# Kernel optimization log

Hardware: AMD Instinct MI355X
Metric: run time of the kernel (lower is better)

Reference implementation:

```python
import jax, jax.numpy as jnp
import numpy as np

N = 50000
E = 800000
IN_DIM = 128
HID = 32
HEADS = 4
NEG_SLOPE = 0.2


def setup_inputs() -> dict:
    key = jax.random.key(0)
    ks = jax.random.split(key, 12)
    x = jax.random.normal(ks[0], (N, IN_DIM), dtype=jnp.float32)
    edge_index = jax.random.randint(ks[1], (2, E), 0, N, dtype=jnp.int64)
    s1 = 1.0 / np.sqrt(IN_DIM)
    s2 = 1.0 / np.sqrt(HEADS * HID)
    W1 = jax.random.normal(ks[2], (IN_DIM, HEADS * HID), dtype=jnp.float32) * s1
    a_src1 = jax.random.normal(ks[3], (HEADS, HID), dtype=jnp.float32) * s1
    a_dst1 = jax.random.normal(ks[4], (HEADS, HID), dtype=jnp.float32) * s1
    b1 = jnp.zeros((HEADS * HID,), dtype=jnp.float32)
    W2 = jax.random.normal(ks[5], (HEADS * HID, HID), dtype=jnp.float32) * s2
    a_src2 = jax.random.normal(ks[6], (1, HID), dtype=jnp.float32) * s2
    a_dst2 = jax.random.normal(ks[7], (1, HID), dtype=jnp.float32) * s2
    b2 = jnp.zeros((HID,), dtype=jnp.float32)
    return {"x": x, "edge_index": edge_index, "W1": W1, "a_src1": a_src1,
            "a_dst1": a_dst1, "b1": b1, "W2": W2, "a_src2": a_src2,
            "a_dst2": a_dst2, "b2": b2}


def _gat_layer(x, W, a_src, a_dst, bias, src, dst, heads, ch):
    n = x.shape[0]
    h = (x @ W).reshape(n, heads, ch)                    # [N,H,C]
    # per-node attention halves (GATv1): a_src . h_i, a_dst . h_j
    al_s = jnp.einsum('nhc,hc->nh', h, a_src)            # [N,H]
    al_d = jnp.einsum('nhc,hc->nh', h, a_dst)
    e = jax.nn.leaky_relu(al_s[src] + al_d[dst], NEG_SLOPE)  # [E,H]
    # segment softmax over edges sharing the same destination
    e_max = jax.ops.segment_max(e, dst, num_segments=n)
    e_exp = jnp.exp(e - e_max[dst])
    denom = jax.ops.segment_sum(e_exp, dst, num_segments=n)
    alpha = e_exp / (denom[dst] + 1e-16)                 # [E,H]
    msg = h[src] * alpha[:, :, None]                     # [E,H,C]
    out = jax.ops.segment_sum(msg, dst, num_segments=n)  # [N,H,C]
    return out.reshape(n, heads * ch) + bias


def reference(x, edge_index, W1, a_src1, a_dst1, b1, W2, a_src2, a_dst2, b2):
    n = x.shape[0]
    # PyG GATConv adds self-loops by default
    loops = jnp.arange(n, dtype=edge_index.dtype)
    src = jnp.concatenate([edge_index[0], loops])
    dst = jnp.concatenate([edge_index[1], loops])
    h = _gat_layer(x, W1, a_src1, a_dst1, b1, src, dst, HEADS, HID)
    h = jax.nn.elu(h)
    out = _gat_layer(h, W2, a_src2, a_dst2, b2, src, dst, 1, HID)
    return out
```

## Files before the change

### kernel.cpp

```cpp
#include <hip/hip_runtime.h>
#include <hip/hip_bf16.h>

#define NN 50000
#define EE 800000
#define EN (EE + NN)
#define IN_DIM 128
#define HID 32
#define HEADS 4
#define F1 (HEADS * HID)
#define NEG 0.2f

typedef __hip_bfloat16 bf16;
typedef __bf16 bf16x8 __attribute__((ext_vector_type(8)));
typedef float f32x4 __attribute__((ext_vector_type(4)));

__device__ __forceinline__ float cvt(float v) { return v; }
__device__ __forceinline__ float cvt(bf16 v)  { return __bfloat162float(v); }

__device__ __forceinline__ float bflo(unsigned u) {
    union { unsigned u; float f; } v; v.u = u << 16; return v.f;
}
__device__ __forceinline__ float bfhi(unsigned u) {
    union { unsigned u; float f; } v; v.u = u & 0xFFFF0000u; return v.f;
}

__device__ __forceinline__ unsigned short f2bf_bits(float f) {
    union { float f; unsigned u; } v; v.f = f;
    unsigned r = v.u + 0x7FFFu + ((v.u >> 16) & 1u);
    return (unsigned short)(r >> 16);
}

__device__ __forceinline__ unsigned short f2h_bits(float f) {
    _Float16 h = (_Float16)f;
    union { _Float16 h; unsigned short s; } v; v.h = h; return v.s;
}
__device__ __forceinline__ float h2f(unsigned short s) {
    union { _Float16 h; unsigned short s; } v; v.s = s; return (float)v.h;
}

__global__ void k_flags(const void* xv, const void* eiv, int* __restrict__ flags) {
    const int t = threadIdx.x;
    const unsigned* xw = (const unsigned*)xv;
    const unsigned* ew = (const unsigned*)eiv;
    int lo_nz = 0, huge = 0, hi_nz = 0;
    for (int j = 0; j < 4; ++j) {
        unsigned w = xw[t * 4 + j];
        unsigned lo = w & 0xFFFFu;
        if (lo != 0u) lo_nz = 1;
        if (((lo >> 7) & 0xFFu) >= 0xC0u) huge = 1;
        unsigned eo = ew[(t * 4 + j) * 2 + 1];
        if (eo != 0u) hi_nz = 1;
    }
    unsigned long long m_lo = __ballot(lo_nz);
    unsigned long long m_hg = __ballot(huge);
    unsigned long long m_hi = __ballot(hi_nz);
    if (t == 0) {
        flags[0] = (m_lo == 0ull || m_hg != 0ull) ? 1 : 0;
        flags[1] = (m_hi == 0ull) ? 1 : 0;
    }
}

template <typename IT>
__device__ __forceinline__ void get_sd(const IT* __restrict__ ei, int idx, int& s, int& d) {
    if (idx < EE) { s = (int)ei[idx]; d = (int)ei[EE + idx]; }
    else          { s = d = idx - EE; }
}
template <typename IT>
__device__ __forceinline__ int dst_of(const IT* __restrict__ ei, int idx) {
    return idx < EE ? (int)ei[EE + idx] : idx - EE;
}

#define HIST_B ((EN + 255) / 256)

__global__ void k_hist(const void* ei, const int* __restrict__ flags,
                       int* __restrict__ counts, int* __restrict__ rank,
                       const void* W1v, const void* W2v,
                       unsigned short* __restrict__ W1T,
                       unsigned short* __restrict__ W2T) {
    if (blockIdx.x >= HIST_B) {
        const int b = blockIdx.x - HIST_B;
        const int t = threadIdx.x;
        const int f32in = flags[0];
        if (b < 16) {
            const unsigned short* wg = (const unsigned short*)W1v;
            const float* wf = (const float*)W1v;
            for (int i = 0; i < 4; ++i) {
                int j = b * 1024 + i * 256 + t;
                int k = j >> 7, n = j & 127;
                W1T[n * 128 + k] = f32in ? f2bf_bits(wf[j]) : wg[j];
            }
        } else {
            const unsigned short* wg = (const unsigned short*)W2v;
            const float* wf = (const float*)W2v;
            for (int i = 0; i < 4; ++i) {
                int j = (b - 16) * 1024 + i * 256 + t;
                int k = j >> 5, n = j & 31;
                W2T[n * 128 + k] = f32in ? f2bf_bits(wf[j]) : wg[j];
            }
        }
        return;
    }
    int idx = blockIdx.x * 256 + threadIdx.x;
    if (idx >= EN) return;
    int d = flags[1] ? dst_of<long long>((const long long*)ei, idx)
                     : dst_of<int>((const int*)ei, idx);
    rank[idx] = atomicAdd(&counts[d], 1);
}

#define SCAN_B 196

__global__ void k_scanA(const int* __restrict__ counts, int* __restrict__ bsum) {
    __shared__ int sh[256];
    int i = blockIdx.x * 256 + threadIdx.x;
    sh[threadIdx.x] = (i < NN) ? counts[i] : 0;
    __syncthreads();
    for (int off = 128; off > 0; off >>= 1) {
        if (threadIdx.x < off) sh[threadIdx.x] += sh[threadIdx.x + off];
        __syncthreads();
    }
    if (threadIdx.x == 0) bsum[blockIdx.x] = sh[0];
}

__global__ void k_scanC(const int* __restrict__ counts, const int* __restrict__ bsum,
                        int* __restrict__ offsets) {
    __shared__ int red[256];
    __shared__ int sh[256];
    const int t = threadIdx.x, b = blockIdx.x;
    red[t] = (t < b) ? bsum[t] : 0;
    __syncthreads();
    for (int off = 128; off > 0; off >>= 1) {
        if (t < off) red[t] += red[t + off];
        __syncthreads();
    }
    const int base = red[0];
    int i = b * 256 + t;
    int v = (i < NN) ? counts[i] : 0;
    sh[t] = v;
    __syncthreads();
    for (int off = 1; off < 256; off <<= 1) {
        int u = (t >= off) ? sh[t - off] : 0;
        __syncthreads();
        sh[t] += u;
        __syncthreads();
    }
    if (i < NN) {
        offsets[i] = base + sh[t] - v;
    } else if (i == NN) {
        offsets[NN] = EN;
    }
}

__global__ void k_scatter(const void* ei, const int* __restrict__ flags,
                          const int* __restrict__ offsets, const int* __restrict__ rank,
                          int* __restrict__ srcs) {
    int idx = blockIdx.x * blockDim.x + threadIdx.x;
    if (idx >= EN) return;
    int s, d;
    if (flags[1]) get_sd<long long>((const long long*)ei, idx, s, d);
    else          get_sd<int>((const int*)ei, idx, s, d);
    int slot = offsets[d] + rank[idx];
    srcs[slot] = s;
}

#define MROWS 64
#define LDK 136

__global__ __launch_bounds__(256) void k_lin1_mfma(
    const void* xv, const unsigned short* __restrict__ W1T,
    const void* as1v, const void* ad1v,
    const int* __restrict__ flags, unsigned* __restrict__ h1,
    float* __restrict__ als, float* __restrict__ ald)
{
    __shared__ __align__(16) char smem[(MROWS + 128) * LDK * 2];
    unsigned short* xs  = (unsigned short*)smem;
    unsigned short* w1t = xs + MROWS * LDK;
    float* hs = (float*)smem;
    __shared__ float sa[F1], sd[F1];

    const int t = threadIdx.x;
    const int row0 = blockIdx.x * MROWS;
    const int f32in = flags[0];

    if (t < F1) {
        sa[t] = f32in ? ((const float*)as1v)[t] : cvt(((const bf16*)as1v)[t]);
        sd[t] = f32in ? ((const float*)ad1v)[t] : cvt(((const bf16*)ad1v)[t]);
    }
    if (!f32in) {
        const uint4* xg = (const uint4*)xv;
        for (int i = 0; i < 4; ++i) {
            int id = i * 256 + t;
            int m = id >> 4, seg = id & 15;
            int gr = row0 + m;
            uint4 val = (gr < NN) ? xg[(size_t)gr * 16 + seg] : make_uint4(0, 0, 0, 0);
            *(uint4*)&xs[m * LDK + seg * 8] = val;
        }
    } else {
        const float4* xf = (const float4*)xv;
        for (int i = 0; i < 8; ++i) {
            int id = i * 256 + t;
            int m = id >> 5, c = id & 31;
            int gr = row0 + m;
            float4 v = (gr < NN) ? xf[(size_t)gr * 32 + c]
                                 : make_float4(0.f, 0.f, 0.f, 0.f);
            unsigned w0 = (unsigned)f2bf_bits(v.x) | ((unsigned)f2bf_bits(v.y) << 16);
            unsigned w1 = (unsigned)f2bf_bits(v.z) | ((unsigned)f2bf_bits(v.w) << 16);
            *(uint2*)&xs[m * LDK + c * 4] = make_uint2(w0, w1);
        }
    }
    {
        const uint4* wg = (const uint4*)W1T;
        for (int i = 0; i < 8; ++i) {
            int id = i * 256 + t;
            int n = id >> 4, seg = id & 15;
            *(uint4*)&w1t[n * LDK + seg * 8] = wg[id];
        }
    }
    __syncthreads();

    const int wave = t >> 6, lane = t & 63, quad = lane >> 4, l16 = lane & 15;
    f32x4 acc[8];
#pragma unroll
    for (int ni = 0; ni < 8; ++ni) acc[ni] = (f32x4){0.f, 0.f, 0.f, 0.f};

    const int arow = wave * 16 + l16;
#pragma unroll
    for (int kc = 0; kc < 4; ++kc) {
        int ko = kc * 32 + quad * 8;
        bf16x8 av = *(const bf16x8*)&xs[arow * LDK + ko];
#pragma unroll
        for (int ni = 0; ni < 8; ++ni) {
            bf16x8 bv = *(const bf16x8*)&w1t[(ni * 16 + l16) * LDK + ko];
            acc[ni] = __builtin_amdgcn_mfma_f32_16x16x32_bf16(av, bv, acc[ni], 0, 0, 0);
        }
    }
    __syncthreads();

#pragma unroll
    for (int ni = 0; ni < 8; ++ni)
#pragma unroll
        for (int r = 0; r < 4; ++r) {
            int m = wave * 16 + quad * 4 + r;
            hs[m * 132 + ni * 16 + l16] = acc[ni][r];
        }
    __syncthreads();

    for (int i = 0; i < 16; ++i) {
        int id = i * 256 + t;
        int m = id >> 6, wd = id & 63;
        int gr = row0 + m;
        if (gr < NN) {
            unsigned pw = (unsigned)f2bf_bits(hs[m * 132 + 2 * wd]) |
                          ((unsigned)f2bf_bits(hs[m * 132 + 2 * wd + 1]) << 16);
            h1[(size_t)gr * 64 + wd] = pw;
        }
    }
    {
        int m = t >> 2, h = t & 3;
        int gr = row0 + m;
        if (gr < NN) {
            float ps = 0.f, pd = 0.f;
#pragma unroll
            for (int j = 0; j < 32; ++j) {
                float v = hs[m * 132 + h * 32 + j];
                ps += v * sa[h * 32 + j];
                pd += v * sd[h * 32 + j];
            }
            als[gr * 4 + h] = ps;
            ald[gr * 4 + h] = pd;
        }
    }
}

__global__ __launch_bounds__(256) void k_agg1(
    const int* __restrict__ offsets, const int* __restrict__ srcs,
    const float* __restrict__ als, const float* __restrict__ ald,
    const bf16* __restrict__ h1, const void* b1v, const int* __restrict__ flags,
    uint2* __restrict__ hm)
{
    const int lane = threadIdx.x & 63;
    const int d = blockIdx.x * 4 + (threadIdx.x >> 6);
    const int q = lane >> 5;
    const int u = lane & 31;
    const int h = u >> 3;
    const int start = offsets[d], end = offsets[d + 1];
    const uint2* rows = (const uint2*)h1;
    const float advh = ald[d * 4 + h];

    float A0[4] = {0,0,0,0}, A1[4] = {0,0,0,0}, A2[4] = {0,0,0,0}, A3[4] = {0,0,0,0};
    float D[4] = {0,0,0,0};
    int e = start + q;
    for (; e + 6 < end; e += 8) {
        int s0 = srcs[e],     s1 = srcs[e + 2];
        int s2 = srcs[e + 4], s3 = srcs[e + 6];
        float e0 = als[s0 * 4 + h] + advh;
        float e1 = als[s1 * 4 + h] + advh;
        float e2 = als[s2 * 4 + h] + advh;
        float e3 = als[s3 * 4 + h] + advh;
        e0 = e0 > 0.f ? e0 : NEG * e0;
        e1 = e1 > 0.f ? e1 : NEG * e1;
        e2 = e2 > 0.f ? e2 : NEG * e2;
        e3 = e3 > 0.f ? e3 : NEG * e3;
        float x0 = __expf(e0), x1 = __expf(e1);
        float x2 = __expf(e2), x3 = __expf(e3);
        uint2 u0 = rows[(size_t)s0 * 32 + u], u1 = rows[(size_t)s1 * 32 + u];
        uint2 u2 = rows[(size_t)s2 * 32 + u], u3 = rows[(size_t)s3 * 32 + u];
        A0[0] += x0 * bflo(u0.x); A0[1] += x0 * bfhi(u0.x);
        A0[2] += x0 * bflo(u0.y); A0[3] += x0 * bfhi(u0.y); D[0] += x0;
        A1[0] += x1 * bflo(u1.x); A1[1] += x1 * bfhi(u1.x);
        A1[2] += x1 * bflo(u1.y); A1[3] += x1 * bfhi(u1.y); D[1] += x1;
        A2[0] += x2 * bflo(u2.x); A2[1] += x2 * bfhi(u2.x);
        A2[2] += x2 * bflo(u2.y); A2[3] += x2 * bfhi(u2.y); D[2] += x2;
        A3[0] += x3 * bflo(u3.x); A3[1] += x3 * bfhi(u3.x);
        A3[2] += x3 * bflo(u3.y); A3[3] += x3 * bfhi(u3.y); D[3] += x3;
    }
    for (; e < end; e += 2) {
        int s0 = srcs[e];
        float e0 = als[s0 * 4 + h] + advh;
        e0 = e0 > 0.f ? e0 : NEG * e0;
        float x0 = __expf(e0);
        uint2 u0 = rows[(size_t)s0 * 32 + u];
        A0[0] += x0 * bflo(u0.x); A0[1] += x0 * bfhi(u0.x);
        A0[2] += x0 * bflo(u0.y); A0[3] += x0 * bfhi(u0.y); D[0] += x0;
    }
    float a0 = A0[0] + A1[0] + A2[0] + A3[0];
    float a1 = A0[1] + A1[1] + A2[1] + A3[1];
    float a2 = A0[2] + A1[2] + A2[2] + A3[2];
    float a3 = A0[3] + A1[3] + A2[3] + A3[3];
    float dsum = D[0] + D[1] + D[2] + D[3];
    a0 += __shfl_xor(a0, 32); a1 += __shfl_xor(a1, 32);
    a2 += __shfl_xor(a2, 32); a3 += __shfl_xor(a3, 32);
    dsum += __shfl_xor(dsum, 32);
    if (q == 0) {
        float inv = 1.f / (dsum + 1e-16f);
        float bb0, bb1, bb2, bb3;
        if (flags[0]) {
            float4 bb = ((const float4*)b1v)[u];
            bb0 = bb.x; bb1 = bb.y; bb2 = bb.z; bb3 = bb.w;
        } else {
            uint2 ub = ((const uint2*)b1v)[u];
            bb0 = bflo(ub.x); bb1 = bfhi(ub.x); bb2 = bflo(ub.y); bb3 = bfhi(ub.y);
        }
        float v0 = a0 * inv + bb0, v1 = a1 * inv + bb1;
        float v2 = a2 * inv + bb2, v3 = a3 * inv + bb3;
        v0 = v0 > 0.f ? v0 : (__expf(v0) - 1.f);
        v1 = v1 > 0.f ? v1 : (__expf(v1) - 1.f);
        v2 = v2 > 0.f ? v2 : (__expf(v2) - 1.f);
        v3 = v3 > 0.f ? v3 : (__expf(v3) - 1.f);
        unsigned w0 = (unsigned)f2bf_bits(v0) | ((unsigned)f2bf_bits(v1) << 16);
        unsigned w1 = (unsigned)f2bf_bits(v2) | ((unsigned)f2bf_bits(v3) << 16);
        hm[(size_t)d * 32 + u] = make_uint2(w0, w1);
    }
}

__global__ __launch_bounds__(256) void k_mid_mfma(
    const bf16* __restrict__ hm, const unsigned short* __restrict__ W2T,
    const void* as2v, const void* ad2v,
    const int* __restrict__ flags, unsigned short* __restrict__ h2,
    float* __restrict__ als2, float* __restrict__ ald2)
{
    __shared__ __align__(16) unsigned short hs[MROWS * LDK];
    __shared__ __align__(16) unsigned short w2t[32 * LDK];
    __shared__ float sa2[HID], sd2[HID];

    const int t = threadIdx.x;
    const int row0 = blockIdx.x * MROWS;
    const int f32in = flags[0];

    if (t < HID) {
        sa2[t] = f32in ? ((const float*)as2v)[t] : cvt(((const bf16*)as2v)[t]);
        sd2[t] = f32in ? ((const float*)ad2v)[t] : cvt(((const bf16*)ad2v)[t]);
    }
    {
        const uint4* hg = (const uint4*)hm;
        for (int i = 0; i < 4; ++i) {
            int id = i * 256 + t;
            int m = id >> 4, seg = id & 15;
            int gr = row0 + m;
            uint4 val = (gr < NN) ? hg[(size_t)gr * 16 + seg] : make_uint4(0, 0, 0, 0);
            *(uint4*)&hs[m * LDK + seg * 8] = val;
        }
        const uint4* wg = (const uint4*)W2T;
        for (int i = 0; i < 2; ++i) {
            int id = i * 256 + t;
            int n = id >> 4, seg = id & 15;
            *(uint4*)&w2t[n * LDK + seg * 8] = wg[id];
        }
    }
    __syncthreads();

    const int wave = t >> 6, lane = t & 63, quad = lane >> 4, l16 = lane & 15;
    f32x4 acc[2];
    acc[0] = (f32x4){0.f, 0.f, 0.f, 0.f};
    acc[1] = (f32x4){0.f, 0.f, 0.f, 0.f};
    const int arow = wave * 16 + l16;
#pragma unroll
    for (int kc = 0; kc < 4; ++kc) {
        int ko = kc * 32 + quad * 8;
        bf16x8 av = *(const bf16x8*)&hs[arow * LDK + ko];
#pragma unroll
        for (int ni = 0; ni < 2; ++ni) {
            bf16x8 bv = *(const bf16x8*)&w2t[(ni * 16 + l16) * LDK + ko];
            acc[ni] = __builtin_amdgcn_mfma_f32_16x16x32_bf16(av, bv, acc[ni], 0, 0, 0);
        }
    }

#pragma unroll
    for (int ni = 0; ni < 2; ++ni)
#pragma unroll
        for (int r = 0; r < 4; ++r) {
            int gr = row0 + wave * 16 + quad * 4 + r;
            if (gr < NN) h2[(size_t)gr * 32 + ni * 16 + l16] = f2h_bits(acc[ni][r]);
        }

    float ps[4], pd[4];
#pragma unroll
    for (int r = 0; r < 4; ++r) {
        ps[r] = acc[0][r] * sa2[l16] + acc[1][r] * sa2[16 + l16];
        pd[r] = acc[0][r] * sd2[l16] + acc[1][r] * sd2[16 + l16];
    }
#pragma unroll
    for (int mask = 1; mask < 16; mask <<= 1)
#pragma unroll
        for (int r = 0; r < 4; ++r) {
            ps[r] += __shfl_xor(ps[r], mask);
            pd[r] += __shfl_xor(pd[r], mask);
        }
    if (l16 == 0) {
#pragma unroll
        for (int r = 0; r < 4; ++r) {
            int gr = row0 + wave * 16 + quad * 4 + r;
            if (gr < NN) { als2[gr] = ps[r]; ald2[gr] = pd[r]; }
        }
    }
}

__global__ __launch_bounds__(256) void k_agg2(
    const int* __restrict__ offsets, const int* __restrict__ srcs,
    const float* __restrict__ als2, const float* __restrict__ ald2,
    const unsigned* __restrict__ h2,
    const void* b2v, const int* __restrict__ flags, void* out)
{
    const int lane = threadIdx.x & 63;
    const int node = blockIdx.x * 4 + (threadIdx.x >> 6);
    const int q = lane >> 4;
    const int u = lane & 15;
    const int start = offsets[node], end = offsets[node + 1];
    const float adv = ald2[node];

    float A0 = 0.f, A1 = 0.f, B0 = 0.f, B1 = 0.f, D0 = 0.f, D1 = 0.f;
    int e = start + q;
    for (; e + 4 < end; e += 8) {
        int s0 = srcs[e], s1 = srcs[e + 4];
        float e0 = als2[s0] + adv, e1 = als2[s1] + adv;
        e0 = e0 > 0.f ? e0 : NEG * e0;
        e1 = e1 > 0.f ? e1 : NEG * e1;
        float x0 = __expf(e0), x1 = __expf(e1);
        unsigned w0 = h2[s0 * 16 + u];
        unsigned w1 = h2[s1 * 16 + u];
        A0 += x0 * h2f((unsigned short)(w0 & 0xFFFFu));
        A1 += x0 * h2f((unsigned short)(w0 >> 16));  D0 += x0;
        B0 += x1 * h2f((unsigned short)(w1 & 0xFFFFu));
        B1 += x1 * h2f((unsigned short)(w1 >> 16));  D1 += x1;
    }
    for (; e < end; e += 4) {
        int s0 = srcs[e];
        float e0 = als2[s0] + adv;
        e0 = e0 > 0.f ? e0 : NEG * e0;
        float x0 = __expf(e0);
        unsigned w0 = h2[s0 * 16 + u];
        A0 += x0 * h2f((unsigned short)(w0 & 0xFFFFu));
        A1 += x0 * h2f((unsigned short)(w0 >> 16));  D0 += x0;
    }
    float a0 = A0 + B0, a1 = A1 + B1, dsum = D0 + D1;
    a0 += __shfl_xor(a0, 16); a1 += __shfl_xor(a1, 16); dsum += __shfl_xor(dsum, 16);
    a0 += __shfl_xor(a0, 32); a1 += __shfl_xor(a1, 32); dsum += __shfl_xor(dsum, 32);
    if (q == 0) {
        float inv = 1.f / (dsum + 1e-16f);
        float r0 = a0 * inv, r1 = a1 * inv;
        if (flags[0]) {
            float2 bb = ((const float2*)b2v)[u];
            ((float2*)out)[(size_t)node * 16 + u] = make_float2(r0 + bb.x, r1 + bb.y);
        } else {
            unsigned ub = ((const unsigned*)b2v)[u];
            r0 += bflo(ub); r1 += bfhi(ub);
            ((unsigned*)out)[(size_t)node * 16 + u] =
                (unsigned)f2bf_bits(r0) | ((unsigned)f2bf_bits(r1) << 16);
        }
    }
}

extern "C" void kernel_launch(void* const* d_in, const int* in_sizes, int n_in,
                              void* d_out, int out_size, void* d_ws, size_t ws_size,
                              hipStream_t stream) {
    const void* x    = d_in[0];
    const void* ei   = d_in[1];
    const void* W1   = d_in[2];
    const void* a_s1 = d_in[3];
    const void* a_d1 = d_in[4];
    const void* b1   = d_in[5];
    const void* W2   = d_in[6];
    const void* a_s2 = d_in[7];
    const void* a_d2 = d_in[8];
    const void* b2v  = d_in[9];

    int*   flags  = (int*)d_ws;
    char*  pc     = (char*)d_ws + 256;
    uint2* hm     = (uint2*)pc;            pc += (size_t)NN * 32 * 8;
    int*   rank   = (int*)hm;
    bf16*  h1     = (bf16*)pc;             pc += (size_t)NN * F1 * 2;
    unsigned short* h2 = (unsigned short*)h1;
    int*   srcs   = (int*)pc;              pc += (size_t)EN * 4;
    float* al_s1  = (float*)pc;            pc += (size_t)NN * HEADS * 4;
    float* al_d1  = (float*)pc;            pc += (size_t)NN * HEADS * 4;
    float* al_s2  = (float*)pc;            pc += (size_t)NN * 4;
    float* al_d2  = (float*)pc;            pc += (size_t)NN * 4;
    int*   offs   = (int*)pc;              pc += (size_t)(NN + 4) * 4;
    int*   counts = (int*)pc;              pc += (size_t)NN * 4;
    unsigned short* W1T = (unsigned short*)pc; pc += (size_t)128 * 128 * 2;
    unsigned short* W2T = (unsigned short*)pc; pc += (size_t)32 * 128 * 2;
    int*   bsum   = (int*)pc;              pc += SCAN_B * 4;

    hipMemsetAsync(counts, 0, (size_t)NN * sizeof(int), stream);

    k_flags<<<1, 64, 0, stream>>>(x, ei, flags);
    k_hist<<<HIST_B + 20, 256, 0, stream>>>(ei, flags, counts, rank, W1, W2, W1T, W2T);
    k_scanA<<<SCAN_B, 256, 0, stream>>>(counts, bsum);
    k_scanC<<<SCAN_B, 256, 0, stream>>>(counts, bsum, offs);
    k_scatter<<<(EN + 255) / 256, 256, 0, stream>>>(ei, flags, offs, rank, srcs);
    k_lin1_mfma<<<(NN + MROWS - 1) / MROWS, 256, 0, stream>>>(x, W1T, a_s1, a_d1,
                                                              flags, (unsigned*)h1,
                                                              al_s1, al_d1);
    k_agg1<<<NN / 4, 256, 0, stream>>>(offs, srcs, al_s1, al_d1, h1, b1, flags, hm);
    k_mid_mfma<<<(NN + MROWS - 1) / MROWS, 256, 0, stream>>>((const bf16*)hm, W2T, a_s2,
                                                             a_d2, flags, h2, al_s2, al_d2);
    k_agg2<<<NN / 4, 256, 0, stream>>>(offs, srcs, al_s2, al_d2, (const unsigned*)h2,
                                       b2v, flags, d_out);
}
```

Before: 228.4 us.

## Merge CSR-build prep kernels, single-block scan, two edges per thread

The memset, flag-detection kernel and weight transposition are folded into one k_prep launch, and each weight block recomputes the input-format flag locally. The two-pass block scan becomes a single 1024-thread block that scans 50 counts per thread. The histogram and scatter kernels now handle two edges per thread with vectorized index loads. Together these cut the launch count and index-load overhead, but the single-block scan runs serially on one CU and its per-thread strided count reads are uncoalesced.

```diff
diff --git a/kernel.cpp b/kernel.cpp
--- a/kernel.cpp
+++ b/kernel.cpp
@@ -38,128 +38,156 @@
     union { _Float16 h; unsigned short s; } v; v.s = s; return (float)v.h;
 }
 
-__global__ void k_flags(const void* xv, const void* eiv, int* __restrict__ flags) {
-    const int t = threadIdx.x;
-    const unsigned* xw = (const unsigned*)xv;
-    const unsigned* ew = (const unsigned*)eiv;
-    int lo_nz = 0, huge = 0, hi_nz = 0;
-    for (int j = 0; j < 4; ++j) {
-        unsigned w = xw[t * 4 + j];
-        unsigned lo = w & 0xFFFFu;
-        if (lo != 0u) lo_nz = 1;
-        if (((lo >> 7) & 0xFFu) >= 0xC0u) huge = 1;
-        unsigned eo = ew[(t * 4 + j) * 2 + 1];
-        if (eo != 0u) hi_nz = 1;
-    }
-    unsigned long long m_lo = __ballot(lo_nz);
-    unsigned long long m_hg = __ballot(huge);
-    unsigned long long m_hi = __ballot(hi_nz);
-    if (t == 0) {
-        flags[0] = (m_lo == 0ull || m_hg != 0ull) ? 1 : 0;
-        flags[1] = (m_hi == 0ull) ? 1 : 0;
-    }
-}
-
-template <typename IT>
-__device__ __forceinline__ void get_sd(const IT* __restrict__ ei, int idx, int& s, int& d) {
-    if (idx < EE) { s = (int)ei[idx]; d = (int)ei[EE + idx]; }
-    else          { s = d = idx - EE; }
-}
-template <typename IT>
-__device__ __forceinline__ int dst_of(const IT* __restrict__ ei, int idx) {
-    return idx < EE ? (int)ei[EE + idx] : idx - EE;
-}
-
-#define HIST_B ((EN + 255) / 256)
-
-__global__ void k_hist(const void* ei, const int* __restrict__ flags,
-                       int* __restrict__ counts, int* __restrict__ rank,
+#define ZERO_B ((NN + 255) / 256)
+#define PREP_B (1 + ZERO_B + 16 + 1)
+
+__global__ void k_prep(const void* xv, const void* eiv,
                        const void* W1v, const void* W2v,
+                       int* __restrict__ flags, int* __restrict__ counts,
                        unsigned short* __restrict__ W1T,
                        unsigned short* __restrict__ W2T) {
-    if (blockIdx.x >= HIST_B) {
-        const int b = blockIdx.x - HIST_B;
-        const int t = threadIdx.x;
-        const int f32in = flags[0];
-        if (b < 16) {
-            const unsigned short* wg = (const unsigned short*)W1v;
-            const float* wf = (const float*)W1v;
-            for (int i = 0; i < 4; ++i) {
-                int j = b * 1024 + i * 256 + t;
-                int k = j >> 7, n = j & 127;
-                W1T[n * 128 + k] = f32in ? f2bf_bits(wf[j]) : wg[j];
+    const int b = blockIdx.x, t = threadIdx.x;
+    if (b == 0) {
+        if (t < 64) {
+            const unsigned* xw = (const unsigned*)xv;
+            const unsigned* ew = (const unsigned*)eiv;
+            int lo_nz = 0, huge = 0, hi_nz = 0;
+            for (int j = 0; j < 4; ++j) {
+                unsigned w = xw[t * 4 + j];
+                unsigned lo = w & 0xFFFFu;
+                if (lo != 0u) lo_nz = 1;
+                if (((lo >> 7) & 0xFFu) >= 0xC0u) huge = 1;
+                unsigned eo = ew[(t * 4 + j) * 2 + 1];
+                if (eo != 0u) hi_nz = 1;
             }
-        } else {
-            const unsigned short* wg = (const unsigned short*)W2v;
-            const float* wf = (const float*)W2v;
-            for (int i = 0; i < 4; ++i) {
-                int j = (b - 16) * 1024 + i * 256 + t;
-                int k = j >> 5, n = j & 31;
-                W2T[n * 128 + k] = f32in ? f2bf_bits(wf[j]) : wg[j];
+            unsigned long long m_lo = __ballot(lo_nz);
+            unsigned long long m_hg = __ballot(huge);
+            unsigned long long m_hi = __ballot(hi_nz);
+            if (t == 0) {
+                flags[0] = (m_lo == 0ull || m_hg != 0ull) ? 1 : 0;
+                flags[1] = (m_hi == 0ull) ? 1 : 0;
             }
         }
         return;
     }
-    int idx = blockIdx.x * 256 + threadIdx.x;
-    if (idx >= EN) return;
-    int d = flags[1] ? dst_of<long long>((const long long*)ei, idx)
-                     : dst_of<int>((const int*)ei, idx);
-    rank[idx] = atomicAdd(&counts[d], 1);
-}
-
-#define SCAN_B 196
-
-__global__ void k_scanA(const int* __restrict__ counts, int* __restrict__ bsum) {
-    __shared__ int sh[256];
-    int i = blockIdx.x * 256 + threadIdx.x;
-    sh[threadIdx.x] = (i < NN) ? counts[i] : 0;
+    if (b <= ZERO_B) {
+        int i = (b - 1) * 256 + t;
+        if (i < NN) counts[i] = 0;
+        return;
+    }
+    __shared__ int sf;
+    if (t < 64) {
+        const unsigned* xw = (const unsigned*)xv;
+        int lo_nz = 0, huge = 0;
+        for (int j = 0; j < 4; ++j) {
+            unsigned w = xw[t * 4 + j];
+            unsigned lo = w & 0xFFFFu;
+            if (lo != 0u) lo_nz = 1;
+            if (((lo >> 7) & 0xFFu) >= 0xC0u) huge = 1;
+        }
+        unsigned long long m_lo = __ballot(lo_nz);
+        unsigned long long m_hg = __ballot(huge);
+        if (t == 0) sf = (m_lo == 0ull || m_hg != 0ull) ? 1 : 0;
+    }
     __syncthreads();
-    for (int off = 128; off > 0; off >>= 1) {
-        if (threadIdx.x < off) sh[threadIdx.x] += sh[threadIdx.x + off];
+    const int f32in = sf;
+    const int tb = b - 1 - ZERO_B;
+    if (tb < 16) {
+        const unsigned short* wg = (const unsigned short*)W1v;
+        const float* wf = (const float*)W1v;
+        for (int i = 0; i < 4; ++i) {
+            int j = tb * 1024 + i * 256 + t;
+            int k = j >> 7, n = j & 127;
+            W1T[n * 128 + k] = f32in ? f2bf_bits(wf[j]) : wg[j];
+        }
+    } else {
+        const unsigned short* wg = (const unsigned short*)W2v;
+        const float* wf = (const float*)W2v;
+        for (int i = 0; i < 16; ++i) {
+            int j = i * 256 + t;
+            int k = j >> 5, n = j & 31;
+            W2T[n * 128 + k] = f32in ? f2bf_bits(wf[j]) : wg[j];
+        }
+    }
+}
+
+#define PAIR_B ((EN / 2 + 255) / 256)
+
+__global__ void k_hist(const void* ei, const int* __restrict__ flags,
+                       int* __restrict__ counts, int* __restrict__ rank) {
+    int p = blockIdx.x * 256 + threadIdx.x;
+    int i2 = p * 2;
+    if (i2 >= EN) return;
+    int d0, d1;
+    if (i2 >= EE) { d0 = i2 - EE; d1 = d0 + 1; }
+    else if (flags[1]) {
+        const long long* e64 = (const long long*)ei;
+        long2 dd = *(const long2*)&e64[EE + i2];
+        d0 = (int)dd.x; d1 = (int)dd.y;
+    } else {
+        const int* e32 = (const int*)ei;
+        int2 dd = *(const int2*)&e32[EE + i2];
+        d0 = dd.x; d1 = dd.y;
+    }
+    int r0 = atomicAdd(&counts[d0], 1);
+    int r1 = atomicAdd(&counts[d1], 1);
+    *(int2*)&rank[i2] = make_int2(r0, r1);
+}
+
+#define SCAN_T 1024
+#define SCAN_PER 50
+
+__global__ __launch_bounds__(1024) void k_scan(const int* __restrict__ counts,
+                                               int* __restrict__ offsets) {
+    __shared__ int part[SCAN_T];
+    const int t = threadIdx.x;
+    const int base = t * SCAN_PER;
+    int sum = 0;
+    for (int j = 0; j < SCAN_PER; ++j) {
+        int i = base + j;
+        sum += (i < NN) ? counts[i] : 0;
+    }
+    part[t] = sum;
+    __syncthreads();
+    for (int off = 1; off < SCAN_T; off <<= 1) {
+        int u = (t >= off) ? part[t - off] : 0;
         __syncthreads();
-    }
-    if (threadIdx.x == 0) bsum[blockIdx.x] = sh[0];
-}
-
-__global__ void k_scanC(const int* __restrict__ counts, const int* __restrict__ bsum,
-                        int* __restrict__ offsets) {
-    __shared__ int red[256];
-    __shared__ int sh[256];
-    const int t = threadIdx.x, b = blockIdx.x;
-    red[t] = (t < b) ? bsum[t] : 0;
-    __syncthreads();
-    for (int off = 128; off > 0; off >>= 1) {
-        if (t < off) red[t] += red[t + off];
+        part[t] += u;
         __syncthreads();
     }
-    const int base = red[0];
-    int i = b * 256 + t;
-    int v = (i < NN) ? counts[i] : 0;
-    sh[t] = v;
-    __syncthreads();
-    for (int off = 1; off < 256; off <<= 1) {
-        int u = (t >= off) ? sh[t - off] : 0;
-        __syncthreads();
-        sh[t] += u;
-        __syncthreads();
-    }
-    if (i < NN) {
-        offsets[i] = base + sh[t] - v;
-    } else if (i == NN) {
-        offsets[NN] = EN;
-    }
+    int run = (t == 0) ? 0 : part[t - 1];
+    for (int j = 0; j < SCAN_PER; ++j) {
+        int i = base + j;
+        if (i < NN) {
+            offsets[i] = run;
+            run += counts[i];
+        }
+    }
+    if (t == SCAN_T - 1) offsets[NN] = EN;
 }
 
 __global__ void k_scatter(const void* ei, const int* __restrict__ flags,
                           const int* __restrict__ offsets, const int* __restrict__ rank,
                           int* __restrict__ srcs) {
-    int idx = blockIdx.x * blockDim.x + threadIdx.x;
-    if (idx >= EN) return;
-    int s, d;
-    if (flags[1]) get_sd<long long>((const long long*)ei, idx, s, d);
-    else          get_sd<int>((const int*)ei, idx, s, d);
-    int slot = offsets[d] + rank[idx];
-    srcs[slot] = s;
+    int p = blockIdx.x * 256 + threadIdx.x;
+    int i2 = p * 2;
+    if (i2 >= EN) return;
+    int s0, s1, d0, d1;
+    if (i2 >= EE) { s0 = d0 = i2 - EE; s1 = d1 = s0 + 1; }
+    else if (flags[1]) {
+        const long long* e64 = (const long long*)ei;
+        long2 ss = *(const long2*)&e64[i2];
+        long2 dd = *(const long2*)&e64[EE + i2];
+        s0 = (int)ss.x; s1 = (int)ss.y; d0 = (int)dd.x; d1 = (int)dd.y;
+    } else {
+        const int* e32 = (const int*)ei;
+        int2 ss = *(const int2*)&e32[i2];
+        int2 dd = *(const int2*)&e32[EE + i2];
+        s0 = ss.x; s1 = ss.y; d0 = dd.x; d1 = dd.y;
+    }
+    int2 rr = *(const int2*)&rank[i2];
+    srcs[offsets[d0] + rr.x] = s0;
+    srcs[offsets[d1] + rr.y] = s1;
 }
 
 #define MROWS 64
@@ -518,15 +546,11 @@
     int*   counts = (int*)pc;              pc += (size_t)NN * 4;
     unsigned short* W1T = (unsigned short*)pc; pc += (size_t)128 * 128 * 2;
     unsigned short* W2T = (unsigned short*)pc; pc += (size_t)32 * 128 * 2;
-    int*   bsum   = (int*)pc;              pc += SCAN_B * 4;
-
-    hipMemsetAsync(counts, 0, (size_t)NN * sizeof(int), stream);
-
-    k_flags<<<1, 64, 0, stream>>>(x, ei, flags);
-    k_hist<<<HIST_B + 20, 256, 0, stream>>>(ei, flags, counts, rank, W1, W2, W1T, W2T);
-    k_scanA<<<SCAN_B, 256, 0, stream>>>(counts, bsum);
-    k_scanC<<<SCAN_B, 256, 0, stream>>>(counts, bsum, offs);
-    k_scatter<<<(EN + 255) / 256, 256, 0, stream>>>(ei, flags, offs, rank, srcs);
+
+    k_prep<<<PREP_B, 256, 0, stream>>>(x, ei, W1, W2, flags, counts, W1T, W2T);
+    k_hist<<<PAIR_B, 256, 0, stream>>>(ei, flags, counts, rank);
+    k_scan<<<1, SCAN_T, 0, stream>>>(counts, offs);
+    k_scatter<<<PAIR_B, 256, 0, stream>>>(ei, flags, offs, rank, srcs);
     k_lin1_mfma<<<(NN + MROWS - 1) / MROWS, 256, 0, stream>>>(x, W1T, a_s1, a_d1,
                                                               flags, (unsigned*)h1,
                                                               al_s1, al_d1);
```

After: 308.9 us. 35.2% more time.
